# Kernel tuning notes

Measured on AMD Instinct MI355X. Metric: run time of the kernel, lower is better.

The kernel has to match this reference:

```python
import jax, jax.numpy as jnp
import numpy as np

B, IN, OUT = 256, 1024, 1024


def choquet_cardinal(z):
    """Discrete Choquet integral over last axis with cardinality measure mu(A)=|A|/n.
    ChI(x) = sum_i (x_(i) - x_(i-1)) * mu(A_i), x_(0)=0, mu(A_i)=(n-i+1)/n.
    """
    n = z.shape[-1]
    xs = jnp.sort(z, axis=-1)  # ascending
    # diffs[..., 0] = x_(1); diffs[..., i] = x_(i+1) - x_(i)
    diffs = jnp.concatenate([xs[..., :1], jnp.diff(xs, axis=-1)], axis=-1)
    mu = (n - jnp.arange(n, dtype=xs.dtype)) / n  # 1, (n-1)/n, ..., 1/n
    return jnp.einsum('...i,i->...', diffs, mu)


def setup_inputs() -> dict:
    key = jax.random.key(0)
    kx, kw, kb = jax.random.split(key, 3)
    x = jax.random.normal(kx, (B, 1, IN), dtype=jnp.float32)
    weight = jax.random.normal(kw, (IN, OUT), dtype=jnp.float32) * 0.02
    bias = jax.random.normal(kb, (IN, OUT), dtype=jnp.float32) * 0.02
    return {"x": x, "weight": weight, "bias": bias}


def reference(x, weight, bias):
    # z: [B, OUT, IN] = x * W^T + b^T (elementwise with broadcast)
    z = x * weight.T + bias.T
    chi = choquet_cardinal(z)  # [B, OUT]
    return jax.nn.sigmoid(chi)
```

## Files before the change

### kernel.cpp

```cpp
#include <hip/hip_runtime.h>
#include <math.h>


#define BATCH   256
#define IN_DIM  1024
#define OUT_DIM 1024

#define TM 64
#define TN 32
#define TK 64

#define ALD 72
#define BLD 72

typedef __bf16 bf16x8 __attribute__((ext_vector_type(8)));
typedef float  f32x4  __attribute__((ext_vector_type(4)));

__global__ __launch_bounds__(256) void chadaline_kernel(
    const float* __restrict__ x,
    const float* __restrict__ w,
    const float* __restrict__ bias,
    float* __restrict__ out)
{
    __shared__ __bf16 Alds[TM * ALD];
    __shared__ __bf16 Blds[TN * BLD];
    __shared__ float  bias_red[8][TN];
    __shared__ float  colsum[TN];

    const int t    = threadIdx.x;
    const int lane = t & 63;
    const int wave = t >> 6;
    const int quad = lane >> 4;
    const int l16  = lane & 15;

    const int bm = blockIdx.y * TM;
    const int on = blockIdx.x * TN;

    const int am = t >> 2;
    const int ak = (t & 3) * 16;
    const int bn = t & 31;
    const int bk = (t >> 5) * 8;

    float bias_acc = 0.f;
    f32x4 acc0 = {0.f, 0.f, 0.f, 0.f};
    f32x4 acc1 = {0.f, 0.f, 0.f, 0.f};

    for (int k0 = 0; k0 < IN_DIM; k0 += TK) {
        const float* xa = x + (size_t)(bm + am) * IN_DIM + k0 + ak;
        const float4 a0 = *(const float4*)(xa + 0);
        const float4 a1 = *(const float4*)(xa + 4);
        const float4 a2 = *(const float4*)(xa + 8);
        const float4 a3 = *(const float4*)(xa + 12);
        bf16x8 v0, v1;
        v0[0] = (__bf16)a0.x; v0[1] = (__bf16)a0.y; v0[2] = (__bf16)a0.z; v0[3] = (__bf16)a0.w;
        v0[4] = (__bf16)a1.x; v0[5] = (__bf16)a1.y; v0[6] = (__bf16)a1.z; v0[7] = (__bf16)a1.w;
        v1[0] = (__bf16)a2.x; v1[1] = (__bf16)a2.y; v1[2] = (__bf16)a2.z; v1[3] = (__bf16)a2.w;
        v1[4] = (__bf16)a3.x; v1[5] = (__bf16)a3.y; v1[6] = (__bf16)a3.z; v1[7] = (__bf16)a3.w;
        *(bf16x8*)(&Alds[am * ALD + ak])     = v0;
        *(bf16x8*)(&Alds[am * ALD + ak + 8]) = v1;

        const float* wb = w + (size_t)(k0 + bk) * OUT_DIM + on + bn;
        bf16x8 bv;
        #pragma unroll
        for (int j = 0; j < 8; ++j) bv[j] = (__bf16)wb[(size_t)j * OUT_DIM];
        *(bf16x8*)(&Blds[bn * BLD + bk]) = bv;

        const float* bb = bias + (size_t)(k0 + bk) * OUT_DIM + on + bn;
        #pragma unroll
        for (int j = 0; j < 8; ++j) bias_acc += bb[(size_t)j * OUT_DIM];

        __syncthreads();

        const __bf16* abase  = &Alds[(wave * 16 + l16) * ALD + quad * 8];
        const __bf16* bbase0 = &Blds[(l16) * BLD + quad * 8];
        const __bf16* bbase1 = &Blds[(16 + l16) * BLD + quad * 8];
        #pragma unroll
        for (int s = 0; s < 2; ++s) {
            bf16x8 af  = *(const bf16x8*)(abase  + s * 32);
            bf16x8 bf0 = *(const bf16x8*)(bbase0 + s * 32);
            bf16x8 bf1 = *(const bf16x8*)(bbase1 + s * 32);
            acc0 = __builtin_amdgcn_mfma_f32_16x16x32_bf16(af, bf0, acc0, 0, 0, 0);
            acc1 = __builtin_amdgcn_mfma_f32_16x16x32_bf16(af, bf1, acc1, 0, 0, 0);
        }
        __syncthreads();
    }

    bias_red[t >> 5][t & 31] = bias_acc;
    __syncthreads();
    if (t < TN) {
        float s = 0.f;
        #pragma unroll
        for (int r = 0; r < 8; ++r) s += bias_red[r][t];
        colsum[t] = s;
    }
    __syncthreads();

    const float inv_n = 1.0f / (float)IN_DIM;
    #pragma unroll
    for (int j = 0; j < 2; ++j) {
        f32x4 a = (j == 0) ? acc0 : acc1;
        const int   col = on + j * 16 + l16;
        const float cs  = colsum[j * 16 + l16];
        #pragma unroll
        for (int r = 0; r < 4; ++r) {
            const int row = bm + wave * 16 + quad * 4 + r;
            const float v = (a[r] + cs) * inv_n;
            out[(size_t)row * OUT_DIM + col] = 1.0f / (1.0f + __expf(-v));
        }
    }
}

extern "C" void kernel_launch(void* const* d_in, const int* in_sizes, int n_in,
                              void* d_out, int out_size, void* d_ws, size_t ws_size,
                              hipStream_t stream) {
    const float* x  = (const float*)d_in[0];
    const float* w  = (const float*)d_in[1];
    const float* b  = (const float*)d_in[2];
    float* out = (float*)d_out;

    dim3 grid(OUT_DIM / TN, BATCH / TM);
    chadaline_kernel<<<grid, 256, 0, stream>>>(x, w, b, out);
}
```

Measured before the change: 74.21 us.

## Retile GEMM to 32x32x256 with register prefetch and float2 loads

Shrinks the M tile to 32 and grows the K tile to 256, doubling the grid so more compute units are busy and cutting the number of barrier-separated K iterations. Next-tile x and W values are prefetched into registers while the current tile is written to LDS. W and bias are read as float2 pairs for wider coalesced access. The trade-off is more register pressure and duplicated bias reads across the extra blocks.

```diff
diff --git a/kernel.cpp b/kernel.cpp
--- a/kernel.cpp
+++ b/kernel.cpp
@@ -6,12 +6,11 @@
 #define IN_DIM  1024
 #define OUT_DIM 1024
 
-#define TM 64
+#define TM 32
 #define TN 32
-#define TK 64
-
-#define ALD 72
-#define BLD 72
+#define TK 256
+#define KITERS (IN_DIM / TK)
+#define LDK (TK + 8)
 
 typedef __bf16 bf16x8 __attribute__((ext_vector_type(8)));
 typedef float  f32x4  __attribute__((ext_vector_type(4)));
@@ -22,91 +21,121 @@
     const float* __restrict__ bias,
     float* __restrict__ out)
 {
-    __shared__ __bf16 Alds[TM * ALD];
-    __shared__ __bf16 Blds[TN * BLD];
-    __shared__ float  bias_red[8][TN];
-    __shared__ float  colsum[TN];
+    __shared__ __bf16 Alds[TM * LDK];
+    __shared__ __bf16 Blds[TN * LDK];
+    __shared__ float  bias_red[16][TN];
 
     const int t    = threadIdx.x;
     const int lane = t & 63;
-    const int wave = t >> 6;
+    const int wv   = t >> 6;
     const int quad = lane >> 4;
     const int l16  = lane & 15;
+    const int tm   = wv & 1;
+    const int tn   = wv >> 1;
 
     const int bm = blockIdx.y * TM;
     const int on = blockIdx.x * TN;
 
-    const int am = t >> 2;
-    const int ak = (t & 3) * 16;
-    const int bn = t & 31;
-    const int bk = (t >> 5) * 8;
+    const int arow  = t >> 3;
+    const int acol0 = (t & 7) * 16;
+    const int np    = t & 15;
+    const int kg    = t >> 4;
 
-    float bias_acc = 0.f;
-    f32x4 acc0 = {0.f, 0.f, 0.f, 0.f};
-    f32x4 acc1 = {0.f, 0.f, 0.f, 0.f};
+    const float* xrow = x    + (size_t)(bm + arow) * IN_DIM + acol0;
+    const float* wcol = w    + (size_t)(kg * 16) * OUT_DIM + on + 2 * np;
+    const float* bcol = bias + (size_t)(kg * 16) * OUT_DIM + on + 2 * np;
 
-    for (int k0 = 0; k0 < IN_DIM; k0 += TK) {
-        const float* xa = x + (size_t)(bm + am) * IN_DIM + k0 + ak;
-        const float4 a0 = *(const float4*)(xa + 0);
-        const float4 a1 = *(const float4*)(xa + 4);
-        const float4 a2 = *(const float4*)(xa + 8);
-        const float4 a3 = *(const float4*)(xa + 12);
-        bf16x8 v0, v1;
-        v0[0] = (__bf16)a0.x; v0[1] = (__bf16)a0.y; v0[2] = (__bf16)a0.z; v0[3] = (__bf16)a0.w;
-        v0[4] = (__bf16)a1.x; v0[5] = (__bf16)a1.y; v0[6] = (__bf16)a1.z; v0[7] = (__bf16)a1.w;
-        v1[0] = (__bf16)a2.x; v1[1] = (__bf16)a2.y; v1[2] = (__bf16)a2.z; v1[3] = (__bf16)a2.w;
-        v1[4] = (__bf16)a3.x; v1[5] = (__bf16)a3.y; v1[6] = (__bf16)a3.z; v1[7] = (__bf16)a3.w;
-        *(bf16x8*)(&Alds[am * ALD + ak])     = v0;
-        *(bf16x8*)(&Alds[am * ALD + ak + 8]) = v1;
+    float4 ra[8];
+    float2 rw[16];
 
-        const float* wb = w + (size_t)(k0 + bk) * OUT_DIM + on + bn;
-        bf16x8 bv;
+    #pragma unroll
+    for (int i = 0; i < 2; ++i)
         #pragma unroll
-        for (int j = 0; j < 8; ++j) bv[j] = (__bf16)wb[(size_t)j * OUT_DIM];
-        *(bf16x8*)(&Blds[bn * BLD + bk]) = bv;
+        for (int jj = 0; jj < 4; ++jj)
+            ra[i * 4 + jj] = *(const float4*)(xrow + i * 128 + jj * 4);
+    #pragma unroll
+    for (int j = 0; j < 16; ++j)
+        rw[j] = *(const float2*)(wcol + (size_t)j * OUT_DIM);
 
-        const float* bb = bias + (size_t)(k0 + bk) * OUT_DIM + on + bn;
+    f32x4 acc = {0.f, 0.f, 0.f, 0.f};
+    float bx = 0.f, by = 0.f;
+
+    for (int it = 0; it < KITERS; ++it) {
         #pragma unroll
-        for (int j = 0; j < 8; ++j) bias_acc += bb[(size_t)j * OUT_DIM];
+        for (int i = 0; i < 2; ++i) {
+            bf16x8 v0, v1;
+            const float4 a0 = ra[i * 4 + 0], a1 = ra[i * 4 + 1];
+            const float4 a2 = ra[i * 4 + 2], a3 = ra[i * 4 + 3];
+            v0[0] = (__bf16)a0.x; v0[1] = (__bf16)a0.y; v0[2] = (__bf16)a0.z; v0[3] = (__bf16)a0.w;
+            v0[4] = (__bf16)a1.x; v0[5] = (__bf16)a1.y; v0[6] = (__bf16)a1.z; v0[7] = (__bf16)a1.w;
+            v1[0] = (__bf16)a2.x; v1[1] = (__bf16)a2.y; v1[2] = (__bf16)a2.z; v1[3] = (__bf16)a2.w;
+            v1[4] = (__bf16)a3.x; v1[5] = (__bf16)a3.y; v1[6] = (__bf16)a3.z; v1[7] = (__bf16)a3.w;
+            *(bf16x8*)&Alds[arow * LDK + acol0 + i * 128]     = v0;
+            *(bf16x8*)&Alds[arow * LDK + acol0 + i * 128 + 8] = v1;
+        }
+        #pragma unroll
+        for (int h = 0; h < 2; ++h) {
+            bf16x8 c0, c1;
+            #pragma unroll
+            for (int j = 0; j < 8; ++j) {
+                c0[j] = (__bf16)rw[h * 8 + j].x;
+                c1[j] = (__bf16)rw[h * 8 + j].y;
+            }
+            *(bf16x8*)&Blds[(2 * np + 0) * LDK + kg * 16 + h * 8] = c0;
+            *(bf16x8*)&Blds[(2 * np + 1) * LDK + kg * 16 + h * 8] = c1;
+        }
+
+        if (it + 1 < KITERS) {
+            const float* xn = xrow + (size_t)(it + 1) * TK;
+            #pragma unroll
+            for (int i = 0; i < 2; ++i)
+                #pragma unroll
+                for (int jj = 0; jj < 4; ++jj)
+                    ra[i * 4 + jj] = *(const float4*)(xn + i * 128 + jj * 4);
+            const float* wn = wcol + (size_t)(it + 1) * TK * OUT_DIM;
+            #pragma unroll
+            for (int j = 0; j < 16; ++j)
+                rw[j] = *(const float2*)(wn + (size_t)j * OUT_DIM);
+        }
+
+        {
+            const float* bn = bcol + (size_t)it * TK * OUT_DIM;
+            #pragma unroll
+            for (int j = 0; j < 16; ++j) {
+                const float2 v = *(const float2*)(bn + (size_t)j * OUT_DIM);
+                bx += v.x; by += v.y;
+            }
+        }
 
         __syncthreads();
 
-        const __bf16* abase  = &Alds[(wave * 16 + l16) * ALD + quad * 8];
-        const __bf16* bbase0 = &Blds[(l16) * BLD + quad * 8];
-        const __bf16* bbase1 = &Blds[(16 + l16) * BLD + quad * 8];
+        const __bf16* ab = &Alds[(tm * 16 + l16) * LDK + quad * 8];
+        const __bf16* bb = &Blds[(tn * 16 + l16) * LDK + quad * 8];
         #pragma unroll
-        for (int s = 0; s < 2; ++s) {
-            bf16x8 af  = *(const bf16x8*)(abase  + s * 32);
-            bf16x8 bf0 = *(const bf16x8*)(bbase0 + s * 32);
-            bf16x8 bf1 = *(const bf16x8*)(bbase1 + s * 32);
-            acc0 = __builtin_amdgcn_mfma_f32_16x16x32_bf16(af, bf0, acc0, 0, 0, 0);
-            acc1 = __builtin_amdgcn_mfma_f32_16x16x32_bf16(af, bf1, acc1, 0, 0, 0);
+        for (int s = 0; s < 8; ++s) {
+            bf16x8 af = *(const bf16x8*)(ab + s * 32);
+            bf16x8 bf = *(const bf16x8*)(bb + s * 32);
+            acc = __builtin_amdgcn_mfma_f32_16x16x32_bf16(af, bf, acc, 0, 0, 0);
         }
         __syncthreads();
     }
 
-    bias_red[t >> 5][t & 31] = bias_acc;
-    __syncthreads();
-    if (t < TN) {
-        float s = 0.f;
-        #pragma unroll
-        for (int r = 0; r < 8; ++r) s += bias_red[r][t];
-        colsum[t] = s;
-    }
+    bias_red[kg][2 * np]     = bx;
+    bias_red[kg][2 * np + 1] = by;
     __syncthreads();
 
+    const int c16 = tn * 16 + l16;
+    float cs = 0.f;
+    #pragma unroll
+    for (int r = 0; r < 16; ++r) cs += bias_red[r][c16];
+
     const float inv_n = 1.0f / (float)IN_DIM;
+    const int col = on + c16;
     #pragma unroll
-    for (int j = 0; j < 2; ++j) {
-        f32x4 a = (j == 0) ? acc0 : acc1;
-        const int   col = on + j * 16 + l16;
-        const float cs  = colsum[j * 16 + l16];
-        #pragma unroll
-        for (int r = 0; r < 4; ++r) {
-            const int row = bm + wave * 16 + quad * 4 + r;
-            const float v = (a[r] + cs) * inv_n;
-            out[(size_t)row * OUT_DIM + col] = 1.0f / (1.0f + __expf(-v));
-        }
+    for (int r = 0; r < 4; ++r) {
+        const int row = bm + tm * 16 + quad * 4 + r;
+        const float v = (acc[r] + cs) * inv_n;
+        out[(size_t)row * OUT_DIM + col] = 1.0f / (1.0f + __expf(-v));
     }
 }
 
```

Result: faster. 71.74 us (-3.3%).

## Split into prepack kernel and split-K MFMA GEMM over fragment-packed bf16 operands

Applied to the files above, without the earlier changes.

Adds a prep kernel that converts x and W to bf16 in MFMA fragment order and computes partial bias column sums once, instead of every block redoing the conversion and bias reduction. The GEMM kernel then uses 16x16 output tiles with four waves splitting K, loads fragments straight from global memory without LDS staging, and reduces the four partial tiles through LDS. It costs an extra kernel launch and a round trip of the packed operands through workspace memory.

```diff
diff --git a/kernel.cpp b/kernel.cpp
--- a/kernel.cpp
+++ b/kernel.cpp
@@ -6,108 +6,112 @@
 #define IN_DIM  1024
 #define OUT_DIM 1024
 
-#define TM 64
-#define TN 32
-#define TK 64
+#define APACK_OFF 0
+#define WPACK_OFF (512 * 1024)
+#define BPART_OFF (2560 * 1024)
 
-#define ALD 72
-#define BLD 72
+#define NWTASK_A   512
+#define NWTASK_W  2048
+#define NWTASK_B   256
+#define NBLK_PREP ((NWTASK_A + NWTASK_W + NWTASK_B) / 4)
 
 typedef __bf16 bf16x8 __attribute__((ext_vector_type(8)));
 typedef float  f32x4  __attribute__((ext_vector_type(4)));
 
-__global__ __launch_bounds__(256) void chadaline_kernel(
+__global__ __launch_bounds__(256) void chad_prep(
     const float* __restrict__ x,
     const float* __restrict__ w,
     const float* __restrict__ bias,
-    float* __restrict__ out)
+    unsigned char* __restrict__ ws)
 {
-    __shared__ __bf16 Alds[TM * ALD];
-    __shared__ __bf16 Blds[TN * BLD];
-    __shared__ float  bias_red[8][TN];
-    __shared__ float  colsum[TN];
+    __bf16* apack = (__bf16*)(ws + APACK_OFF);
+    __bf16* wpack = (__bf16*)(ws + WPACK_OFF);
+    float*  bpart = (float*)(ws + BPART_OFF);
 
     const int t    = threadIdx.x;
     const int lane = t & 63;
-    const int wave = t >> 6;
+    const int wv   = t >> 6;
+    const int g    = blockIdx.x * 4 + wv;
+    const int l16  = lane & 15;
     const int quad = lane >> 4;
-    const int l16  = lane & 15;
 
-    const int bm = blockIdx.y * TM;
-    const int on = blockIdx.x * TN;
+    if (g < NWTASK_A) {
+        const int mt = g >> 5, s = g & 31;
+        const float* src = x + (size_t)(mt * 16 + l16) * IN_DIM + s * 32 + quad * 8;
+        const float4 v0 = *(const float4*)src;
+        const float4 v1 = *(const float4*)(src + 4);
+        bf16x8 o;
+        o[0] = (__bf16)v0.x; o[1] = (__bf16)v0.y; o[2] = (__bf16)v0.z; o[3] = (__bf16)v0.w;
+        o[4] = (__bf16)v1.x; o[5] = (__bf16)v1.y; o[6] = (__bf16)v1.z; o[7] = (__bf16)v1.w;
+        *(bf16x8*)(apack + (size_t)g * 512 + lane * 8) = o;
+    } else if (g < NWTASK_A + NWTASK_W) {
+        const int wt = g - NWTASK_A;
+        const int nt = wt >> 5, s = wt & 31;
+        const float* src = w + (size_t)(s * 32 + quad * 8) * OUT_DIM + nt * 16 + l16;
+        bf16x8 o;
+        #pragma unroll
+        for (int j = 0; j < 8; ++j) o[j] = (__bf16)src[(size_t)j * OUT_DIM];
+        *(bf16x8*)(wpack + (size_t)wt * 512 + lane * 8) = o;
+    } else {
+        const int bt = g - NWTASK_A - NWTASK_W;
+        const int rc = bt >> 4, cc = bt & 15;
+        const int col = cc * 64 + lane;
+        const float* src = bias + (size_t)rc * 64 * OUT_DIM + col;
+        float sum = 0.f;
+        #pragma unroll 8
+        for (int r = 0; r < 64; ++r) sum += src[(size_t)r * OUT_DIM];
+        bpart[rc * OUT_DIM + col] = sum;
+    }
+}
 
-    const int am = t >> 2;
-    const int ak = (t & 3) * 16;
-    const int bn = t & 31;
-    const int bk = (t >> 5) * 8;
+__global__ __launch_bounds__(256) void chad_gemm(
+    const unsigned char* __restrict__ ws,
+    float* __restrict__ out)
+{
+    const __bf16* apack = (const __bf16*)(ws + APACK_OFF);
+    const __bf16* wpack = (const __bf16*)(ws + WPACK_OFF);
+    const float*  bpart = (const float*)(ws + BPART_OFF);
 
-    float bias_acc = 0.f;
-    f32x4 acc0 = {0.f, 0.f, 0.f, 0.f};
-    f32x4 acc1 = {0.f, 0.f, 0.f, 0.f};
+    __shared__ float red[4][64][4];
+    __shared__ float cs_lds[16];
 
-    for (int k0 = 0; k0 < IN_DIM; k0 += TK) {
-        const float* xa = x + (size_t)(bm + am) * IN_DIM + k0 + ak;
-        const float4 a0 = *(const float4*)(xa + 0);
-        const float4 a1 = *(const float4*)(xa + 4);
-        const float4 a2 = *(const float4*)(xa + 8);
-        const float4 a3 = *(const float4*)(xa + 12);
-        bf16x8 v0, v1;
-        v0[0] = (__bf16)a0.x; v0[1] = (__bf16)a0.y; v0[2] = (__bf16)a0.z; v0[3] = (__bf16)a0.w;
-        v0[4] = (__bf16)a1.x; v0[5] = (__bf16)a1.y; v0[6] = (__bf16)a1.z; v0[7] = (__bf16)a1.w;
-        v1[0] = (__bf16)a2.x; v1[1] = (__bf16)a2.y; v1[2] = (__bf16)a2.z; v1[3] = (__bf16)a2.w;
-        v1[4] = (__bf16)a3.x; v1[5] = (__bf16)a3.y; v1[6] = (__bf16)a3.z; v1[7] = (__bf16)a3.w;
-        *(bf16x8*)(&Alds[am * ALD + ak])     = v0;
-        *(bf16x8*)(&Alds[am * ALD + ak + 8]) = v1;
+    const int t    = threadIdx.x;
+    const int lane = t & 63;
+    const int wv   = t >> 6;
+    const int mt   = blockIdx.x >> 6;
+    const int nt   = blockIdx.x & 63;
 
-        const float* wb = w + (size_t)(k0 + bk) * OUT_DIM + on + bn;
-        bf16x8 bv;
-        #pragma unroll
-        for (int j = 0; j < 8; ++j) bv[j] = (__bf16)wb[(size_t)j * OUT_DIM];
-        *(bf16x8*)(&Blds[bn * BLD + bk]) = bv;
+    const __bf16* ab = apack + ((size_t)(mt * 32 + wv * 8) * 64 + lane) * 8;
+    const __bf16* bb = wpack + ((size_t)(nt * 32 + wv * 8) * 64 + lane) * 8;
 
-        const float* bb = bias + (size_t)(k0 + bk) * OUT_DIM + on + bn;
-        #pragma unroll
-        for (int j = 0; j < 8; ++j) bias_acc += bb[(size_t)j * OUT_DIM];
-
-        __syncthreads();
-
-        const __bf16* abase  = &Alds[(wave * 16 + l16) * ALD + quad * 8];
-        const __bf16* bbase0 = &Blds[(l16) * BLD + quad * 8];
-        const __bf16* bbase1 = &Blds[(16 + l16) * BLD + quad * 8];
-        #pragma unroll
-        for (int s = 0; s < 2; ++s) {
-            bf16x8 af  = *(const bf16x8*)(abase  + s * 32);
-            bf16x8 bf0 = *(const bf16x8*)(bbase0 + s * 32);
-            bf16x8 bf1 = *(const bf16x8*)(bbase1 + s * 32);
-            acc0 = __builtin_amdgcn_mfma_f32_16x16x32_bf16(af, bf0, acc0, 0, 0, 0);
-            acc1 = __builtin_amdgcn_mfma_f32_16x16x32_bf16(af, bf1, acc1, 0, 0, 0);
-        }
-        __syncthreads();
+    bf16x8 af[8], bfv[8];
+    #pragma unroll
+    for (int i = 0; i < 8; ++i) {
+        af[i]  = *(const bf16x8*)(ab + (size_t)i * 512);
+        bfv[i] = *(const bf16x8*)(bb + (size_t)i * 512);
     }
 
-    bias_red[t >> 5][t & 31] = bias_acc;
-    __syncthreads();
-    if (t < TN) {
+    f32x4 acc = {0.f, 0.f, 0.f, 0.f};
+    #pragma unroll
+    for (int i = 0; i < 8; ++i)
+        acc = __builtin_amdgcn_mfma_f32_16x16x32_bf16(af[i], bfv[i], acc, 0, 0, 0);
+
+    *(f32x4*)&red[wv][lane][0] = acc;
+
+    if (t < 16) {
         float s = 0.f;
         #pragma unroll
-        for (int r = 0; r < 8; ++r) s += bias_red[r][t];
-        colsum[t] = s;
+        for (int p = 0; p < 16; ++p) s += bpart[p * OUT_DIM + nt * 16 + t];
+        cs_lds[t] = s;
     }
     __syncthreads();
 
-    const float inv_n = 1.0f / (float)IN_DIM;
-    #pragma unroll
-    for (int j = 0; j < 2; ++j) {
-        f32x4 a = (j == 0) ? acc0 : acc1;
-        const int   col = on + j * 16 + l16;
-        const float cs  = colsum[j * 16 + l16];
-        #pragma unroll
-        for (int r = 0; r < 4; ++r) {
-            const int row = bm + wave * 16 + quad * 4 + r;
-            const float v = (a[r] + cs) * inv_n;
-            out[(size_t)row * OUT_DIM + col] = 1.0f / (1.0f + __expf(-v));
-        }
-    }
+    const int row = t >> 4, col = t & 15;
+    const int rl  = ((row >> 2) << 4) + col;
+    const int rr  = row & 3;
+    float v = red[0][rl][rr] + red[1][rl][rr] + red[2][rl][rr] + red[3][rl][rr];
+    v = (v + cs_lds[col]) * (1.0f / (float)IN_DIM);
+    out[(size_t)(mt * 16 + row) * OUT_DIM + nt * 16 + col] = 1.0f / (1.0f + __expf(-v));
 }
 
 extern "C" void kernel_launch(void* const* d_in, const int* in_sizes, int n_in,
@@ -118,6 +122,7 @@
     const float* b  = (const float*)d_in[2];
     float* out = (float*)d_out;
 
-    dim3 grid(OUT_DIM / TN, BATCH / TM);
-    chadaline_kernel<<<grid, 256, 0, stream>>>(x, w, b, out);
+    chad_prep<<<NBLK_PREP, 256, 0, stream>>>(x, w, b, (unsigned char*)d_ws);
+    chad_gemm<<<(BATCH / 16) * (OUT_DIM / 16), 256, 0, stream>>>(
+        (const unsigned char*)d_ws, out);
 }
```

New measurement: 70.58 us. 4.9% less time.
